# Kernel optimization log

Hardware: AMD Instinct MI355X
Metric: run time of the kernel (lower is better)

## Reference

```python
import jax, jax.numpy as jnp
import numpy as np

NUM_CLASSES = 10000
NUM_PROXIES = 10
EMB_DIM = 128
MARGIN_DELTA = 0.01
LAMBDA_ = 20.0
GAMMA = 0.1


def setup_inputs() -> dict:
    key = jax.random.key(0)
    k1, k2, k3 = jax.random.split(key, 3)
    features = jax.random.normal(k1, (256, EMB_DIM), dtype=jnp.float32)
    labels = jax.random.randint(k2, (256,), 0, NUM_CLASSES, dtype=jnp.int64)
    # xavier_uniform over (num_classes, num_proxies, emb_dim): fan_in=emb_dim (last dim),
    # fan_out=num_proxies (torch treats dim0 as fan_out-ish for >2D; use standard gain=1)
    fan_in, fan_out = NUM_PROXIES * EMB_DIM, NUM_CLASSES  # torch: fan_in = prod(dims[1:]), fan_out = dims[0]
    limit = float(np.sqrt(6.0 / (fan_in + fan_out)))
    proxies = jax.random.uniform(k3, (NUM_CLASSES, NUM_PROXIES, EMB_DIM),
                                 dtype=jnp.float32, minval=-limit, maxval=limit)
    return {"features": features, "labels": labels, "proxies": proxies}


def reference(features, labels, proxies):
    B = features.shape[0]
    split = B // 2
    # dot_products: [B, C, K]
    dots = jnp.einsum('bd,ckd->bck', features, proxies)
    w = jax.nn.softmax(dots / GAMMA, axis=2)          # softmax over proxies
    S_ic = jnp.sum(w * dots, axis=2)                   # [B, C]
    S_avg = (S_ic[:split] + S_ic[split:]) * 0.5        # [split, C]
    lab = labels[:split]
    idx = jnp.arange(split)
    S_correct = S_avg[idx, lab] - MARGIN_DELTA         # [split]
    S_scaled = LAMBDA_ * S_avg
    S_correct_scaled = LAMBDA_ * S_correct
    S_corrected = S_scaled.at[idx, lab].set(S_correct_scaled)
    denom = jax.nn.logsumexp(S_corrected, axis=1)
    loss = -jnp.mean(S_correct_scaled - denom)
    return loss
```

## Files before the change

kernel.cpp:

```cpp
#include <hip/hip_runtime.h>
#include <hip/hip_bf16.h>

#define NUM_CLASSES 10000
#define NUM_PROXIES 10
#define EMB_DIM 128
#define HALF_B 128
#define MARGIN_DELTA 0.01f
#define LAMBDA_ 20.0f
#define INV_GAMMA 10.0f

#define CB 8
#define ROWS (CB * NUM_PROXIES)
#define MF 5
#define KSTEPS 4
#define TPB 5
#define NBLK 250
#define NTILE 1250
#define TSTRIDE 164

#define SBYTES 40960
#define COFF   (2 * SBYTES)
#define ROFF   (COFF + TSTRIDE * 256)
#define SMEMSZ (ROFF + 1024)

#define GLOBAL_AS __attribute__((address_space(1)))
#define LDS_AS    __attribute__((address_space(3)))

typedef __bf16 bf16x8 __attribute__((ext_vector_type(8)));
typedef float f32x4 __attribute__((ext_vector_type(4)));
typedef unsigned short ushort_t;

__device__ __forceinline__ unsigned int pk2bf(float a, float b) {
    __bf16 ha = (__bf16)a, hb = (__bf16)b;
    return (unsigned int)__builtin_bit_cast(ushort_t, ha) |
           ((unsigned int)__builtin_bit_cast(ushort_t, hb) << 16);
}
__device__ __forceinline__ float bf2f(unsigned int u16) {
    unsigned int x = u16 << 16;
    return __builtin_bit_cast(float, x);
}
__device__ __forceinline__ void dma16(const void* g, void* lds) {
    __builtin_amdgcn_global_load_lds((const GLOBAL_AS void*)g,
                                     (LDS_AS void*)lds, 16, 0, 0);
}

__device__ __forceinline__ void issue_dma(const float* __restrict__ prox,
                                          int tileIdx, char* Sb, int w, int lane) {
    const char* pbase = (const char*)(prox + (size_t)tileIdx * ROWS * EMB_DIM);
    const int dr = lane >> 5;
    const int pc = lane & 31;
    #pragma unroll
    for (int j = 0; j < 10; ++j) {
        int row = w * 20 + 2 * j + dr;
        dma16(pbase + row * 512 + ((pc ^ (row & 7)) << 4),
              Sb + w * 10240 + j * 1024);
    }
}

__device__ __forceinline__ void tile_compute(
    char* smem, const char* Sb, const bf16x8 (&bfrag)[4][KSTEPS],
    int tileIdx, int lab, float* __restrict__ Ps, float* __restrict__ sc,
    int tid, int w, int l15, int g)
{
    f32x4 acc[MF][4];
    #pragma unroll
    for (int mf = 0; mf < MF; ++mf)
        #pragma unroll
        for (int nf = 0; nf < 4; ++nf)
            acc[mf][nf] = (f32x4){0.f, 0.f, 0.f, 0.f};

    #pragma unroll
    for (int t = 0; t < KSTEPS; ++t) {
        #pragma unroll
        for (int mf = 0; mf < MF; ++mf) {
            int row = mf * 16 + l15;
            int s   = row & 7;
            int lc  = 2 * (t * 4 + g);
            float4 a0 = *(const float4*)(Sb + row * 512 + ((lc       ^ s) << 4));
            float4 a1 = *(const float4*)(Sb + row * 512 + (((lc + 1) ^ s) << 4));
            bf16x8 a = (bf16x8){ (__bf16)a0.x, (__bf16)a0.y, (__bf16)a0.z, (__bf16)a0.w,
                                 (__bf16)a1.x, (__bf16)a1.y, (__bf16)a1.z, (__bf16)a1.w };
            #pragma unroll
            for (int nf = 0; nf < 4; ++nf)
                acc[mf][nf] = __builtin_amdgcn_mfma_f32_16x16x32_bf16(
                    a, bfrag[nf][t], acc[mf][nf], 0, 0, 0);
        }
    }

    char* C = smem + COFF;
    #pragma unroll
    for (int mf = 0; mf < MF; ++mf) {
        #pragma unroll
        for (int nf = 0; nf < 4; ++nf) {
            int col  = w * 64 + nf * 16 + l15;
            int rowb = mf * 16 + g * 4;
            unsigned int lo = pk2bf(acc[mf][nf][0], acc[mf][nf][1]);
            unsigned int hi = pk2bf(acc[mf][nf][2], acc[mf][nf][3]);
            char* p = C + col * TSTRIDE + rowb * 2;
            *(unsigned int*)p       = lo;
            *(unsigned int*)(p + 4) = hi;
        }
    }
    asm volatile("s_waitcnt lgkmcnt(0)" ::: "memory");
    __builtin_amdgcn_s_barrier();
    __builtin_amdgcn_sched_barrier(0);

    const int colh  = tid & 127;
    const int chalf = tid >> 7;
    float lsum = 0.f;
    #pragma unroll
    for (int cl4 = 0; cl4 < 4; ++cl4) {
        int cl = chalf * 4 + cl4;
        float Ssum = 0.f;
        #pragma unroll
        for (int h = 0; h < 2; ++h) {
            const char* base = C + (colh + h * 128) * TSTRIDE + cl * 20;
            float d[10];
            #pragma unroll
            for (int p5 = 0; p5 < 5; ++p5) {
                unsigned int pr = *(const unsigned int*)(base + p5 * 4);
                d[2 * p5]     = bf2f(pr & 0xFFFFu);
                d[2 * p5 + 1] = bf2f(pr >> 16);
            }
            float sw = 0.f, sd = 0.f;
            #pragma unroll
            for (int k = 0; k < NUM_PROXIES; ++k) {
                float e = __expf(d[k] * INV_GAMMA);
                sw += e;
                sd += e * d[k];
            }
            Ssum += sd / sw;
        }
        float Savg = 0.5f * Ssum;
        int c = tileIdx * CB + cl;
        float x = LAMBDA_ * Savg;
        if (c == lab) {
            x -= LAMBDA_ * MARGIN_DELTA;
            sc[colh] = x;
        }
        lsum += __expf(x);
    }

    float* rowsum = (float*)(smem + ROFF);
    rowsum[tid] = lsum;
    asm volatile("s_waitcnt lgkmcnt(0)" ::: "memory");
    __builtin_amdgcn_s_barrier();
    __builtin_amdgcn_sched_barrier(0);
    if (tid < HALF_B)
        Ps[(size_t)tileIdx * HALF_B + tid] = rowsum[tid] + rowsum[tid + 128];
}

#define TILE_SYNC(N)                                        \
    asm volatile("s_waitcnt vmcnt(" #N ")" ::: "memory");   \
    __builtin_amdgcn_s_barrier();                           \
    __builtin_amdgcn_sched_barrier(0)

__global__ __launch_bounds__(256, 1) void compute_S_kernel(
    const float* __restrict__ prox,
    const float* __restrict__ feat,
    const int* __restrict__ labels,
    float* __restrict__ Ps,
    float* __restrict__ sc)
{
    __shared__ __align__(16) char smem[SMEMSZ];

    const int tid  = threadIdx.x;
    const int lane = tid & 63;
    const int w    = tid >> 6;
    const int l15  = lane & 15;
    const int g    = lane >> 4;
    const int lab  = labels[tid & 127];

    char* S0 = smem;
    char* S1 = smem + SBYTES;
    const int base = blockIdx.x * TPB;

    bf16x8 bfrag[4][KSTEPS];
    #pragma unroll
    for (int nf = 0; nf < 4; ++nf) {
        #pragma unroll
        for (int t = 0; t < KSTEPS; ++t) {
            int col = w * 64 + nf * 16 + l15;
            const float4* fp = (const float4*)(feat + (size_t)col * EMB_DIM + t * 32 + g * 8);
            float4 v0 = fp[0], v1 = fp[1];
            bfrag[nf][t] = (bf16x8){ (__bf16)v0.x, (__bf16)v0.y, (__bf16)v0.z, (__bf16)v0.w,
                                     (__bf16)v1.x, (__bf16)v1.y, (__bf16)v1.z, (__bf16)v1.w };
        }
    }

    issue_dma(prox, base + 0, S0, w, lane);

    issue_dma(prox, base + 1, S1, w, lane);
    TILE_SYNC(10);
    tile_compute(smem, S0, bfrag, base + 0, lab, Ps, sc, tid, w, l15, g);

    issue_dma(prox, base + 2, S0, w, lane);
    TILE_SYNC(11);
    tile_compute(smem, S1, bfrag, base + 1, lab, Ps, sc, tid, w, l15, g);

    issue_dma(prox, base + 3, S1, w, lane);
    TILE_SYNC(11);
    tile_compute(smem, S0, bfrag, base + 2, lab, Ps, sc, tid, w, l15, g);

    issue_dma(prox, base + 4, S0, w, lane);
    TILE_SYNC(11);
    tile_compute(smem, S1, bfrag, base + 3, lab, Ps, sc, tid, w, l15, g);

    TILE_SYNC(2);
    tile_compute(smem, S0, bfrag, base + 4, lab, Ps, sc, tid, w, l15, g);
}

__global__ __launch_bounds__(256) void psum_kernel(
    const float* __restrict__ Ps,
    float* __restrict__ Psum2)
{
    const int b0  = blockIdx.x * 25;
    const int tid = threadIdx.x;
    const int r   = tid >> 5;
    const int c   = tid & 31;

    float4 s = make_float4(0.f, 0.f, 0.f, 0.f);
    #pragma unroll
    for (int j = 0; j < 4; ++j) {
        int b = r + 8 * j;
        if (b < 25) {
            float4 v = *(const float4*)(Ps + (size_t)(b0 + b) * HALF_B + c * 4);
            s.x += v.x; s.y += v.y; s.z += v.z; s.w += v.w;
        }
    }

    __shared__ float red[8][HALF_B];
    *(float4*)&red[r][c * 4] = s;
    __syncthreads();
    if (tid < HALF_B) {
        float t = 0.f;
        #pragma unroll
        for (int rr = 0; rr < 8; ++rr) t += red[rr][tid];
        Psum2[blockIdx.x * HALF_B + tid] = t;
    }
}

__global__ __launch_bounds__(128) void finalize_kernel(
    const float* __restrict__ Psum2,
    const float* __restrict__ sc,
    float* __restrict__ out)
{
    const int i = threadIdx.x;
    float t = 0.f;
    #pragma unroll
    for (int b = 0; b < 50; ++b) t += Psum2[b * HALF_B + i];
    float part = sc[i] - __logf(t);

    __shared__ float buf[HALF_B];
    buf[i] = part;
    __syncthreads();
    #pragma unroll
    for (int off = 64; off >= 1; off >>= 1) {
        if (i < off) buf[i] += buf[i + off];
        __syncthreads();
    }
    if (i == 0) out[0] = -buf[0] / (float)HALF_B;
}

extern "C" void kernel_launch(void* const* d_in, const int* in_sizes, int n_in,
                              void* d_out, int out_size, void* d_ws, size_t ws_size,
                              hipStream_t stream) {
    const float* feat   = (const float*)d_in[0];
    const int*   labels = (const int*)d_in[1];
    const float* prox   = (const float*)d_in[2];
    float* out = (float*)d_out;

    float* Ps    = (float*)d_ws;
    float* sc    = (float*)((char*)d_ws + 640000);
    float* Psum2 = (float*)((char*)d_ws + 640000 + 512);

    compute_S_kernel<<<NBLK, 256, 0, stream>>>(prox, feat, labels, Ps, sc);
    psum_kernel<<<50, 256, 0, stream>>>(Ps, Psum2);
    finalize_kernel<<<1, 128, 0, stream>>>(Psum2, sc, out);
}
```

Measured before the change: 35.14 us.

## Use one tile per block with register-staged bf16 LDS instead of DMA pipeline

Replaces the 250-block persistent kernel, which double-buffered five tiles per block through global_load_lds DMA in fp32, with 1250 blocks that each handle a single tile. Each block loads its proxies into registers, converts them to bf16 once and stores them swizzled into LDS, so the MFMA A-operand is read with a single 16-byte LDS load. The smaller LDS footprint and launch_bounds(256,2) allow more blocks per CU, letting occupancy hide load latency in place of the explicit software pipeline. The cost is that every block reloads and converts the feature fragments, and there is no overlap of loads and compute within a block. The row-sum scratch is also moved into padding of the C buffer, and s_setprio is added around the MFMA loop.

```diff
diff --git a/kernel.cpp b/kernel.cpp
--- a/kernel.cpp
+++ b/kernel.cpp
@@ -13,20 +13,15 @@
 #define ROWS (CB * NUM_PROXIES)
 #define MF 5
 #define KSTEPS 4
-#define TPB 5
-#define NBLK 250
 #define NTILE 1250
 #define TSTRIDE 164
 
-#define SBYTES 40960
-#define COFF   (2 * SBYTES)
-#define ROFF   (COFF + TSTRIDE * 256)
-#define SMEMSZ (ROFF + 1024)
-
-#define GLOBAL_AS __attribute__((address_space(1)))
-#define LDS_AS    __attribute__((address_space(3)))
+#define SBYTES (ROWS * EMB_DIM * 2)
+#define COFF   SBYTES
+#define SMEMSZ (COFF + TSTRIDE * 256)
 
 typedef __bf16 bf16x8 __attribute__((ext_vector_type(8)));
+typedef __bf16 bf16x4 __attribute__((ext_vector_type(4)));
 typedef float f32x4 __attribute__((ext_vector_type(4)));
 typedef unsigned short ushort_t;
 
@@ -39,29 +34,55 @@
     unsigned int x = u16 << 16;
     return __builtin_bit_cast(float, x);
 }
-__device__ __forceinline__ void dma16(const void* g, void* lds) {
-    __builtin_amdgcn_global_load_lds((const GLOBAL_AS void*)g,
-                                     (LDS_AS void*)lds, 16, 0, 0);
-}
-
-__device__ __forceinline__ void issue_dma(const float* __restrict__ prox,
-                                          int tileIdx, char* Sb, int w, int lane) {
-    const char* pbase = (const char*)(prox + (size_t)tileIdx * ROWS * EMB_DIM);
-    const int dr = lane >> 5;
-    const int pc = lane & 31;
+
+__global__ __launch_bounds__(256, 2) void compute_S_kernel(
+    const float* __restrict__ prox,
+    const float* __restrict__ feat,
+    const int* __restrict__ labels,
+    float* __restrict__ Ps,
+    float* __restrict__ sc)
+{
+    __shared__ __align__(16) char smem[SMEMSZ];
+
+    const int tid     = threadIdx.x;
+    const int lane    = tid & 63;
+    const int w       = tid >> 6;
+    const int l15     = lane & 15;
+    const int g       = lane >> 4;
+    const int tileIdx = blockIdx.x;
+    const int lab     = labels[tid & 127];
+
+    const char* pbase = (const char*)prox + (size_t)tileIdx * (ROWS * EMB_DIM * 4);
+    float4 sv[10];
+    #pragma unroll
+    for (int j = 0; j < 10; ++j)
+        sv[j] = *(const float4*)(pbase + ((size_t)(j * 256 + tid) << 4));
+
+    bf16x8 bfrag[4][KSTEPS];
+    #pragma unroll
+    for (int nf = 0; nf < 4; ++nf) {
+        #pragma unroll
+        for (int t = 0; t < KSTEPS; ++t) {
+            int col = w * 64 + nf * 16 + l15;
+            const float4* fp = (const float4*)(feat + (size_t)col * EMB_DIM + t * 32 + g * 8);
+            float4 v0 = fp[0], v1 = fp[1];
+            bfrag[nf][t] = (bf16x8){ (__bf16)v0.x, (__bf16)v0.y, (__bf16)v0.z, (__bf16)v0.w,
+                                     (__bf16)v1.x, (__bf16)v1.y, (__bf16)v1.z, (__bf16)v1.w };
+        }
+    }
+
     #pragma unroll
     for (int j = 0; j < 10; ++j) {
-        int row = w * 20 + 2 * j + dr;
-        dma16(pbase + row * 512 + ((pc ^ (row & 7)) << 4),
-              Sb + w * 10240 + j * 1024);
-    }
-}
-
-__device__ __forceinline__ void tile_compute(
-    char* smem, const char* Sb, const bf16x8 (&bfrag)[4][KSTEPS],
-    int tileIdx, int lab, float* __restrict__ Ps, float* __restrict__ sc,
-    int tid, int w, int l15, int g)
-{
+        int cid = j * 256 + tid;
+        int row = cid >> 5;
+        int c32 = cid & 31;
+        int off = row * 256 + ((((c32 >> 1) ^ (row & 7))) << 4) + ((c32 & 1) << 3);
+        bf16x4 o = { (__bf16)sv[j].x, (__bf16)sv[j].y, (__bf16)sv[j].z, (__bf16)sv[j].w };
+        *(bf16x4*)(smem + off) = o;
+    }
+
+    __syncthreads();
+
     f32x4 acc[MF][4];
     #pragma unroll
     for (int mf = 0; mf < MF; ++mf)
@@ -69,23 +90,21 @@
         for (int nf = 0; nf < 4; ++nf)
             acc[mf][nf] = (f32x4){0.f, 0.f, 0.f, 0.f};
 
+    __builtin_amdgcn_s_setprio(1);
     #pragma unroll
     for (int t = 0; t < KSTEPS; ++t) {
         #pragma unroll
         for (int mf = 0; mf < MF; ++mf) {
             int row = mf * 16 + l15;
-            int s   = row & 7;
-            int lc  = 2 * (t * 4 + g);
-            float4 a0 = *(const float4*)(Sb + row * 512 + ((lc       ^ s) << 4));
-            float4 a1 = *(const float4*)(Sb + row * 512 + (((lc + 1) ^ s) << 4));
-            bf16x8 a = (bf16x8){ (__bf16)a0.x, (__bf16)a0.y, (__bf16)a0.z, (__bf16)a0.w,
-                                 (__bf16)a1.x, (__bf16)a1.y, (__bf16)a1.z, (__bf16)a1.w };
+            int ck  = (t * 4 + g) ^ (row & 7);
+            bf16x8 a = *(const bf16x8*)(smem + row * 256 + (ck << 4));
             #pragma unroll
             for (int nf = 0; nf < 4; ++nf)
                 acc[mf][nf] = __builtin_amdgcn_mfma_f32_16x16x32_bf16(
                     a, bfrag[nf][t], acc[mf][nf], 0, 0, 0);
         }
     }
+    __builtin_amdgcn_s_setprio(0);
 
     char* C = smem + COFF;
     #pragma unroll
@@ -101,9 +120,7 @@
             *(unsigned int*)(p + 4) = hi;
         }
     }
-    asm volatile("s_waitcnt lgkmcnt(0)" ::: "memory");
-    __builtin_amdgcn_s_barrier();
-    __builtin_amdgcn_sched_barrier(0);
+    __syncthreads();
 
     const int colh  = tid & 127;
     const int chalf = tid >> 7;
@@ -141,73 +158,13 @@
         lsum += __expf(x);
     }
 
-    float* rowsum = (float*)(smem + ROFF);
-    rowsum[tid] = lsum;
-    asm volatile("s_waitcnt lgkmcnt(0)" ::: "memory");
-    __builtin_amdgcn_s_barrier();
-    __builtin_amdgcn_sched_barrier(0);
-    if (tid < HALF_B)
-        Ps[(size_t)tileIdx * HALF_B + tid] = rowsum[tid] + rowsum[tid + 128];
-}
-
-#define TILE_SYNC(N)                                        \
-    asm volatile("s_waitcnt vmcnt(" #N ")" ::: "memory");   \
-    __builtin_amdgcn_s_barrier();                           \
-    __builtin_amdgcn_sched_barrier(0)
-
-__global__ __launch_bounds__(256, 1) void compute_S_kernel(
-    const float* __restrict__ prox,
-    const float* __restrict__ feat,
-    const int* __restrict__ labels,
-    float* __restrict__ Ps,
-    float* __restrict__ sc)
-{
-    __shared__ __align__(16) char smem[SMEMSZ];
-
-    const int tid  = threadIdx.x;
-    const int lane = tid & 63;
-    const int w    = tid >> 6;
-    const int l15  = lane & 15;
-    const int g    = lane >> 4;
-    const int lab  = labels[tid & 127];
-
-    char* S0 = smem;
-    char* S1 = smem + SBYTES;
-    const int base = blockIdx.x * TPB;
-
-    bf16x8 bfrag[4][KSTEPS];
-    #pragma unroll
-    for (int nf = 0; nf < 4; ++nf) {
-        #pragma unroll
-        for (int t = 0; t < KSTEPS; ++t) {
-            int col = w * 64 + nf * 16 + l15;
-            const float4* fp = (const float4*)(feat + (size_t)col * EMB_DIM + t * 32 + g * 8);
-            float4 v0 = fp[0], v1 = fp[1];
-            bfrag[nf][t] = (bf16x8){ (__bf16)v0.x, (__bf16)v0.y, (__bf16)v0.z, (__bf16)v0.w,
-                                     (__bf16)v1.x, (__bf16)v1.y, (__bf16)v1.z, (__bf16)v1.w };
-        }
-    }
-
-    issue_dma(prox, base + 0, S0, w, lane);
-
-    issue_dma(prox, base + 1, S1, w, lane);
-    TILE_SYNC(10);
-    tile_compute(smem, S0, bfrag, base + 0, lab, Ps, sc, tid, w, l15, g);
-
-    issue_dma(prox, base + 2, S0, w, lane);
-    TILE_SYNC(11);
-    tile_compute(smem, S1, bfrag, base + 1, lab, Ps, sc, tid, w, l15, g);
-
-    issue_dma(prox, base + 3, S1, w, lane);
-    TILE_SYNC(11);
-    tile_compute(smem, S0, bfrag, base + 2, lab, Ps, sc, tid, w, l15, g);
-
-    issue_dma(prox, base + 4, S0, w, lane);
-    TILE_SYNC(11);
-    tile_compute(smem, S1, bfrag, base + 3, lab, Ps, sc, tid, w, l15, g);
-
-    TILE_SYNC(2);
-    tile_compute(smem, S0, bfrag, base + 4, lab, Ps, sc, tid, w, l15, g);
+    *(float*)(C + tid * TSTRIDE + 160) = lsum;
+    __syncthreads();
+    if (tid < HALF_B) {
+        float a = *(const float*)(C + tid * TSTRIDE + 160);
+        float b = *(const float*)(C + (tid + 128) * TSTRIDE + 160);
+        Ps[(size_t)tileIdx * HALF_B + tid] = a + b;
+    }
 }
 
 __global__ __launch_bounds__(256) void psum_kernel(
@@ -274,7 +231,7 @@
     float* sc    = (float*)((char*)d_ws + 640000);
     float* Psum2 = (float*)((char*)d_ws + 640000 + 512);
 
-    compute_S_kernel<<<NBLK, 256, 0, stream>>>(prox, feat, labels, Ps, sc);
+    compute_S_kernel<<<NTILE, 256, 0, stream>>>(prox, feat, labels, Ps, sc);
     psum_kernel<<<50, 256, 0, stream>>>(Ps, Psum2);
     finalize_kernel<<<1, 128, 0, stream>>>(Psum2, sc, out);
 }
```

After: 34.52 us. Within noise of the previous version (-1.8%).
